# Kernel optimization log

Measured on AMD Instinct MI355X. Metric: run time of the kernel, lower is better.

## Reference

```python
import jax, jax.numpy as jnp
import numpy as np

N_HEAD = 4

def setup_inputs() -> dict:
    key = jax.random.key(0)
    ks = jax.random.split(key, 5)
    B, T, C = 2, 4096, 64
    return {
        "x": jax.random.normal(ks[0], (B, T, C), dtype=jnp.float32),
        "w_attn": jax.random.normal(ks[1], (3 * C, C), dtype=jnp.float32) * 0.02,
        "b_attn": jax.random.normal(ks[2], (3 * C,), dtype=jnp.float32) * 0.02,
        "w_proj": jax.random.normal(ks[3], (C, C), dtype=jnp.float32) * 0.02,
        "b_proj": jax.random.normal(ks[4], (C,), dtype=jnp.float32) * 0.02,
    }

def reference(x, w_attn, b_attn, w_proj, b_proj):
    B, T, C = x.shape
    H = N_HEAD
    Dh = C // H
    # fused QKV projection (torch Linear: x @ W.T + b)
    qkv = x @ w_attn.T + b_attn                      # [B,T,3C]
    q, k, v = jnp.split(qkv, 3, axis=-1)             # each [B,T,C]
    q = q.reshape(B, T, H, Dh).transpose(0, 2, 1, 3)  # [B,H,T,Dh]
    k = k.reshape(B, T, H, Dh).transpose(0, 2, 1, 3)
    v = v.reshape(B, T, H, Dh).transpose(0, 2, 1, 3)
    scale = 1.0 / np.sqrt(Dh).astype(np.float32)
    scores = jnp.einsum("bhqd,bhkd->bhqk", q, k) * scale  # [B,H,T,T]
    attn = jax.nn.softmax(scores, axis=-1)
    y = jnp.einsum("bhqk,bhkd->bhqd", attn, v)       # [B,H,T,Dh]
    y = y.transpose(0, 2, 1, 3).reshape(B, T, C)     # [B,T,C]
    return y @ w_proj.T + b_proj
```

## Files before the change

kernel.cpp:

```cpp
#include <hip/hip_runtime.h>
#include <math.h>

#define BB 2
#define TT 4096
#define CC 64
#define HH 4
#define DH 16
#define NROW (BB*TT)
#define SCALE 0.36067376022224085f

typedef __fp16 h4 __attribute__((ext_vector_type(4)));
typedef __fp16 h2 __attribute__((ext_vector_type(2)));
typedef float  f4 __attribute__((ext_vector_type(4)));

__global__ __launch_bounds__(256) void qkv_kernel(const float* __restrict__ x,
        const float* __restrict__ w, const float* __restrict__ bias,
        __fp16* __restrict__ Q, __fp16* __restrict__ K, __fp16* __restrict__ VT) {
    __shared__ __fp16 smv[64][16];
    const int t = threadIdx.x;
    const int wave = t >> 6, lane = t & 63;
    const int lq = lane & 15, g = lane >> 4;
    const int r0 = blockIdx.x*16;
    const int b = r0 >> 12, tt0 = r0 & (TT-1);

    h4 xb[4];
    const float* xrow = x + (size_t)(r0 + lq)*CC;
    #pragma unroll
    for (int s = 0; s < 4; s++) {
        float4 xv = *(const float4*)(xrow + s*16 + g*4);
        h2 lo = __builtin_amdgcn_cvt_pkrtz(xv.x, xv.y);
        h2 hi = __builtin_amdgcn_cvt_pkrtz(xv.z, xv.w);
        xb[s] = (h4){lo.x, lo.y, hi.x, hi.y};
    }

    #pragma unroll
    for (int j = 0; j < 3; j++) {
        const int nt = wave*3 + j;
        const int o0 = nt*16;
        const float sc = (nt < 4) ? SCALE : 1.0f;
        float4 bv = *(const float4*)(bias + o0 + g*4);
        f4 acc = {bv.x*sc, bv.y*sc, bv.z*sc, bv.w*sc};
        #pragma unroll
        for (int s = 0; s < 4; s++) {
            float4 wv = *(const float4*)(w + (size_t)(o0 + lq)*CC + s*16 + g*4);
            h2 lo = __builtin_amdgcn_cvt_pkrtz(wv.x*sc, wv.y*sc);
            h2 hi = __builtin_amdgcn_cvt_pkrtz(wv.z*sc, wv.w*sc);
            h4 af = (h4){lo.x, lo.y, hi.x, hi.y};
            acc = __builtin_amdgcn_mfma_f32_16x16x16f16(af, xb[s], acc, 0, 0, 0);
        }
        h2 plo = __builtin_amdgcn_cvt_pkrtz(acc.x, acc.y);
        h2 phi = __builtin_amdgcn_cvt_pkrtz(acc.z, acc.w);
        h4 pk = (h4){plo.x, plo.y, phi.x, phi.y};
        if (nt < 8) {
            const int part = nt >> 2, h = nt & 3;
            __fp16* dst = (part == 0) ? Q : K;
            *(h4*)(dst + ((size_t)(b*HH + h)*TT + tt0 + lq)*DH + g*4) = pk;
        } else {
            const int h = nt - 8;
            smv[h*16 + g*4 + 0][lq] = pk.x;
            smv[h*16 + g*4 + 1][lq] = pk.y;
            smv[h*16 + g*4 + 2][lq] = pk.z;
            smv[h*16 + g*4 + 3][lq] = pk.w;
        }
    }
    __syncthreads();
    if (t < 64) {
        const int h = t >> 4, d = t & 15;
        uint4 v0 = *(const uint4*)&smv[t][0];
        uint4 v1 = *(const uint4*)&smv[t][8];
        __fp16* dst = VT + (size_t)(b*HH + h)*TT*DH
                        + (size_t)((tt0 >> 6)*16 + d)*64 + (tt0 & 63);
        *(uint4*)dst = v0;
        *(uint4*)(dst + 8) = v1;
    }
}

__global__ __launch_bounds__(256) void attn_kernel(const __fp16* __restrict__ Q,
        const __fp16* __restrict__ K, const __fp16* __restrict__ VT,
        __fp16* __restrict__ yh) {
    __shared__ f4    Osm[4][4][64];
    __shared__ float Lsm[4][4][64];
    const int t = threadIdx.x;
    const int wave = t >> 6, lane = t & 63;
    const int lq = lane & 15, g = lane >> 4;
    const int head = blockIdx.x >> 6;
    const int qt   = blockIdx.x & 63;
    const int q0 = qt*64;
    const __fp16* Qh = Q  + (size_t)head*TT*DH;
    const __fp16* Kh = K  + (size_t)head*TT*DH;
    const __fp16* Vh = VT + (size_t)head*TT*DH;

    h4 qf[4];
    #pragma unroll
    for (int h = 0; h < 4; h++)
        qf[h] = *(const h4*)(Qh + (size_t)(q0 + h*16 + lq)*DH + g*4);

    f4 O[4];
    float lp[4];
    #pragma unroll
    for (int h = 0; h < 4; h++) { O[h] = (f4){0.f,0.f,0.f,0.f}; lp[h] = 0.f; }

    const __fp16* kp = Kh + (size_t)(wave*1024 + lq)*DH + g*4;
    const __fp16* vp = Vh + (size_t)(wave*16)*1024 + lq*64 + g*4;

    h4 ka[4], va[4], kb[4], vb[4];
    #pragma unroll
    for (int s = 0; s < 4; s++) {
        ka[s] = *(const h4*)(kp + (size_t)s*16*DH);
        va[s] = *(const h4*)(vp + s*16);
    }

#define ATTN_CHUNK(KF, VF)                                                        \
    {                                                                             \
        const f4 z = {0.f, 0.f, 0.f, 0.f};                                        \
        _Pragma("unroll")                                                         \
        for (int h = 0; h < 4; h++) {                                             \
            f4 S0 = __builtin_amdgcn_mfma_f32_16x16x16f16(KF[0], qf[h], z, 0,0,0);\
            f4 S1 = __builtin_amdgcn_mfma_f32_16x16x16f16(KF[1], qf[h], z, 0,0,0);\
            f4 S2 = __builtin_amdgcn_mfma_f32_16x16x16f16(KF[2], qf[h], z, 0,0,0);\
            f4 S3 = __builtin_amdgcn_mfma_f32_16x16x16f16(KF[3], qf[h], z, 0,0,0);\
            float p0, p1, p2, p3; h2 lo, hi; h4 P; float lacc = 0.f;              \
            p0 = __builtin_amdgcn_exp2f(S0.x); p1 = __builtin_amdgcn_exp2f(S0.y); \
            p2 = __builtin_amdgcn_exp2f(S0.z); p3 = __builtin_amdgcn_exp2f(S0.w); \
            lacc += p0 + p1 + p2 + p3;                                            \
            lo = __builtin_amdgcn_cvt_pkrtz(p0, p1);                              \
            hi = __builtin_amdgcn_cvt_pkrtz(p2, p3);                              \
            P = (h4){lo.x, lo.y, hi.x, hi.y};                                     \
            O[h] = __builtin_amdgcn_mfma_f32_16x16x16f16(VF[0], P, O[h], 0,0,0);  \
            p0 = __builtin_amdgcn_exp2f(S1.x); p1 = __builtin_amdgcn_exp2f(S1.y); \
            p2 = __builtin_amdgcn_exp2f(S1.z); p3 = __builtin_amdgcn_exp2f(S1.w); \
            lacc += p0 + p1 + p2 + p3;                                            \
            lo = __builtin_amdgcn_cvt_pkrtz(p0, p1);                              \
            hi = __builtin_amdgcn_cvt_pkrtz(p2, p3);                              \
            P = (h4){lo.x, lo.y, hi.x, hi.y};                                     \
            O[h] = __builtin_amdgcn_mfma_f32_16x16x16f16(VF[1], P, O[h], 0,0,0);  \
            p0 = __builtin_amdgcn_exp2f(S2.x); p1 = __builtin_amdgcn_exp2f(S2.y); \
            p2 = __builtin_amdgcn_exp2f(S2.z); p3 = __builtin_amdgcn_exp2f(S2.w); \
            lacc += p0 + p1 + p2 + p3;                                            \
            lo = __builtin_amdgcn_cvt_pkrtz(p0, p1);                              \
            hi = __builtin_amdgcn_cvt_pkrtz(p2, p3);                              \
            P = (h4){lo.x, lo.y, hi.x, hi.y};                                     \
            O[h] = __builtin_amdgcn_mfma_f32_16x16x16f16(VF[2], P, O[h], 0,0,0);  \
            p0 = __builtin_amdgcn_exp2f(S3.x); p1 = __builtin_amdgcn_exp2f(S3.y); \
            p2 = __builtin_amdgcn_exp2f(S3.z); p3 = __builtin_amdgcn_exp2f(S3.w); \
            lacc += p0 + p1 + p2 + p3;                                            \
            lo = __builtin_amdgcn_cvt_pkrtz(p0, p1);                              \
            hi = __builtin_amdgcn_cvt_pkrtz(p2, p3);                              \
            P = (h4){lo.x, lo.y, hi.x, hi.y};                                     \
            O[h] = __builtin_amdgcn_mfma_f32_16x16x16f16(VF[3], P, O[h], 0,0,0);  \
            lp[h] += lacc;                                                        \
        }                                                                         \
    }

    for (int step = 0; step < 16; step += 2) {
        {
            const __fp16* kp1 = kp + (size_t)(step + 1)*64*DH;
            const __fp16* vp1 = vp + (size_t)(step + 1)*1024;
            #pragma unroll
            for (int s = 0; s < 4; s++) {
                kb[s] = *(const h4*)(kp1 + (size_t)s*16*DH);
                vb[s] = *(const h4*)(vp1 + s*16);
            }
        }
        ATTN_CHUNK(ka, va)
        {
            const int c2 = (step + 2 < 16) ? step + 2 : 15;
            const __fp16* kp2 = kp + (size_t)c2*64*DH;
            const __fp16* vp2 = vp + (size_t)c2*1024;
            #pragma unroll
            for (int s = 0; s < 4; s++) {
                ka[s] = *(const h4*)(kp2 + (size_t)s*16*DH);
                va[s] = *(const h4*)(vp2 + s*16);
            }
        }
        ATTN_CHUNK(kb, vb)
    }
#undef ATTN_CHUNK

    #pragma unroll
    for (int h = 0; h < 4; h++) {
        Osm[wave][h][lane] = O[h];
        Lsm[wave][h][lane] = lp[h];
    }
    __syncthreads();

    f4 Os = Osm[0][wave][lane];
    Os += Osm[1][wave][lane];
    Os += Osm[2][wave][lane];
    Os += Osm[3][wave][lane];
    float L = 0.f;
    #pragma unroll
    for (int ks = 0; ks < 4; ks++)
        #pragma unroll
        for (int gg = 0; gg < 4; gg++)
            L += Lsm[ks][wave][gg*16 + lq];
    const float rinv = 1.f / L;
    h2 lo = __builtin_amdgcn_cvt_pkrtz(Os.x*rinv, Os.y*rinv);
    h2 hi = __builtin_amdgcn_cvt_pkrtz(Os.z*rinv, Os.w*rinv);
    h4 pk = (h4){lo.x, lo.y, hi.x, hi.y};
    const int b = head >> 2, hh = head & 3;
    *(h4*)(yh + ((size_t)b*TT + q0 + wave*16 + lq)*CC + hh*DH + g*4) = pk;
}

__global__ __launch_bounds__(256) void proj_kernel(const __fp16* __restrict__ yh,
        const float* __restrict__ w, const float* __restrict__ bias,
        float* __restrict__ out) {
    const int t = threadIdx.x;
    const int wave = t >> 6, lane = t & 63;
    const int lq = lane & 15, g = lane >> 4;
    const int r0 = blockIdx.x*16;

    h4 ya[4];
    const __fp16* yrow = yh + (size_t)(r0 + lq)*CC;
    #pragma unroll
    for (int ks = 0; ks < 4; ks++) ya[ks] = *(const h4*)(yrow + ks*16 + g*4);

    const int o = wave*16 + lq;
    const float bv = bias[o];
    f4 acc = {bv, bv, bv, bv};
    #pragma unroll
    for (int ks = 0; ks < 4; ks++) {
        float4 wv = *(const float4*)(w + (size_t)o*CC + ks*16 + g*4);
        h2 lo = __builtin_amdgcn_cvt_pkrtz(wv.x, wv.y);
        h2 hi = __builtin_amdgcn_cvt_pkrtz(wv.z, wv.w);
        h4 bf = (h4){lo.x, lo.y, hi.x, hi.y};
        acc = __builtin_amdgcn_mfma_f32_16x16x16f16(ya[ks], bf, acc, 0, 0, 0);
    }
    #pragma unroll
    for (int reg = 0; reg < 4; reg++)
        out[(size_t)(r0 + g*4 + reg)*CC + o] = acc[reg];
}

extern "C" void kernel_launch(void* const* d_in, const int* in_sizes, int n_in,
                              void* d_out, int out_size, void* d_ws, size_t ws_size,
                              hipStream_t stream) {
    const float* x      = (const float*)d_in[0];
    const float* w_attn = (const float*)d_in[1];
    const float* b_attn = (const float*)d_in[2];
    const float* w_proj = (const float*)d_in[3];
    const float* b_proj = (const float*)d_in[4];
    float* out = (float*)d_out;

    const size_t headsz = (size_t)BB*HH*TT*DH;
    __fp16* Q   = (__fp16*)d_ws;
    __fp16* K   = Q + headsz;
    __fp16* VT  = K + headsz;
    __fp16* yh  = VT + headsz;

    qkv_kernel<<<NROW/16, 256, 0, stream>>>(x, w_attn, b_attn, Q, K, VT);
    attn_kernel<<<BB*HH*(TT/64), 256, 0, stream>>>(Q, K, VT, yh);
    proj_kernel<<<NROW/16, 256, 0, stream>>>(yh, w_proj, b_proj, out);
}
```

Before: 95.33 us.

## Split attention key range across eight waves and vectorize projection output stores

Result: no change. 95.94 us (+0.6%).

```diff
diff --git a/kernel.cpp b/kernel.cpp
--- a/kernel.cpp
+++ b/kernel.cpp
@@ -75,7 +75,7 @@
     }
 }
 
-__global__ __launch_bounds__(256) void attn_kernel(const __fp16* __restrict__ Q,
+__global__ __launch_bounds__(512) void attn_kernel(const __fp16* __restrict__ Q,
         const __fp16* __restrict__ K, const __fp16* __restrict__ VT,
         __fp16* __restrict__ yh) {
     __shared__ f4    Osm[4][4][64];
@@ -100,8 +100,8 @@
     #pragma unroll
     for (int h = 0; h < 4; h++) { O[h] = (f4){0.f,0.f,0.f,0.f}; lp[h] = 0.f; }
 
-    const __fp16* kp = Kh + (size_t)(wave*1024 + lq)*DH + g*4;
-    const __fp16* vp = Vh + (size_t)(wave*16)*1024 + lq*64 + g*4;
+    const __fp16* kp = Kh + (size_t)(wave*512 + lq)*DH + g*4;
+    const __fp16* vp = Vh + (size_t)(wave*8)*1024 + lq*64 + g*4;
 
     h4 ka[4], va[4], kb[4], vb[4];
     #pragma unroll
@@ -152,7 +152,7 @@
         }                                                                         \
     }
 
-    for (int step = 0; step < 16; step += 2) {
+    for (int step = 0; step < 8; step += 2) {
         {
             const __fp16* kp1 = kp + (size_t)(step + 1)*64*DH;
             const __fp16* vp1 = vp + (size_t)(step + 1)*1024;
@@ -164,7 +164,7 @@
         }
         ATTN_CHUNK(ka, va)
         {
-            const int c2 = (step + 2 < 16) ? step + 2 : 15;
+            const int c2 = (step + 2 < 8) ? step + 2 : 7;
             const __fp16* kp2 = kp + (size_t)c2*64*DH;
             const __fp16* vp2 = vp + (size_t)c2*1024;
             #pragma unroll
@@ -177,29 +177,48 @@
     }
 #undef ATTN_CHUNK
 
-    #pragma unroll
-    for (int h = 0; h < 4; h++) {
-        Osm[wave][h][lane] = O[h];
-        Lsm[wave][h][lane] = lp[h];
-    }
-    __syncthreads();
-
-    f4 Os = Osm[0][wave][lane];
-    Os += Osm[1][wave][lane];
-    Os += Osm[2][wave][lane];
-    Os += Osm[3][wave][lane];
-    float L = 0.f;
-    #pragma unroll
-    for (int ks = 0; ks < 4; ks++)
-        #pragma unroll
-        for (int gg = 0; gg < 4; gg++)
-            L += Lsm[ks][wave][gg*16 + lq];
-    const float rinv = 1.f / L;
-    h2 lo = __builtin_amdgcn_cvt_pkrtz(Os.x*rinv, Os.y*rinv);
-    h2 hi = __builtin_amdgcn_cvt_pkrtz(Os.z*rinv, Os.w*rinv);
-    h4 pk = (h4){lo.x, lo.y, hi.x, hi.y};
-    const int b = head >> 2, hh = head & 3;
-    *(h4*)(yh + ((size_t)b*TT + q0 + wave*16 + lq)*CC + hh*DH + g*4) = pk;
+    if (wave >= 4) {
+        #pragma unroll
+        for (int h = 0; h < 4; h++) {
+            Osm[wave-4][h][lane] = O[h];
+            Lsm[wave-4][h][lane] = lp[h];
+        }
+    }
+    __syncthreads();
+    if (wave < 4) {
+        #pragma unroll
+        for (int h = 0; h < 4; h++) {
+            O[h] += Osm[wave][h][lane];
+            lp[h] += Lsm[wave][h][lane];
+        }
+    }
+    __syncthreads();
+    if (wave < 4) {
+        #pragma unroll
+        for (int h = 0; h < 4; h++) {
+            Osm[wave][h][lane] = O[h];
+            Lsm[wave][h][lane] = lp[h];
+        }
+    }
+    __syncthreads();
+    if (wave < 4) {
+        f4 Os = Osm[0][wave][lane];
+        Os += Osm[1][wave][lane];
+        Os += Osm[2][wave][lane];
+        Os += Osm[3][wave][lane];
+        float L = 0.f;
+        #pragma unroll
+        for (int ks = 0; ks < 4; ks++)
+            #pragma unroll
+            for (int gg = 0; gg < 4; gg++)
+                L += Lsm[ks][wave][gg*16 + lq];
+        const float rinv = 1.f / L;
+        h2 lo = __builtin_amdgcn_cvt_pkrtz(Os.x*rinv, Os.y*rinv);
+        h2 hi = __builtin_amdgcn_cvt_pkrtz(Os.z*rinv, Os.w*rinv);
+        h4 pk = (h4){lo.x, lo.y, hi.x, hi.y};
+        const int b = head >> 2, hh = head & 3;
+        *(h4*)(yh + ((size_t)b*TT + q0 + wave*16 + lq)*CC + hh*DH + g*4) = pk;
+    }
 }
 
 __global__ __launch_bounds__(256) void proj_kernel(const __fp16* __restrict__ yh,
@@ -209,26 +228,24 @@
     const int wave = t >> 6, lane = t & 63;
     const int lq = lane & 15, g = lane >> 4;
     const int r0 = blockIdx.x*16;
-
-    h4 ya[4];
+    const int o0 = wave*16;
+
+    h4 yb[4];
     const __fp16* yrow = yh + (size_t)(r0 + lq)*CC;
     #pragma unroll
-    for (int ks = 0; ks < 4; ks++) ya[ks] = *(const h4*)(yrow + ks*16 + g*4);
-
-    const int o = wave*16 + lq;
-    const float bv = bias[o];
-    f4 acc = {bv, bv, bv, bv};
-    #pragma unroll
-    for (int ks = 0; ks < 4; ks++) {
-        float4 wv = *(const float4*)(w + (size_t)o*CC + ks*16 + g*4);
+    for (int s = 0; s < 4; s++) yb[s] = *(const h4*)(yrow + s*16 + g*4);
+
+    float4 bv = *(const float4*)(bias + o0 + g*4);
+    f4 acc = {bv.x, bv.y, bv.z, bv.w};
+    #pragma unroll
+    for (int s = 0; s < 4; s++) {
+        float4 wv = *(const float4*)(w + (size_t)(o0 + lq)*CC + s*16 + g*4);
         h2 lo = __builtin_amdgcn_cvt_pkrtz(wv.x, wv.y);
         h2 hi = __builtin_amdgcn_cvt_pkrtz(wv.z, wv.w);
-        h4 bf = (h4){lo.x, lo.y, hi.x, hi.y};
-        acc = __builtin_amdgcn_mfma_f32_16x16x16f16(ya[ks], bf, acc, 0, 0, 0);
-    }
-    #pragma unroll
-    for (int reg = 0; reg < 4; reg++)
-        out[(size_t)(r0 + g*4 + reg)*CC + o] = acc[reg];
+        h4 af = (h4){lo.x, lo.y, hi.x, hi.y};
+        acc = __builtin_amdgcn_mfma_f32_16x16x16f16(af, yb[s], acc, 0, 0, 0);
+    }
+    *(float4*)(out + (size_t)(r0 + lq)*CC + o0 + g*4) = (float4){acc.x, acc.y, acc.z, acc.w};
 }
 
 extern "C" void kernel_launch(void* const* d_in, const int* in_sizes, int n_in,
@@ -248,6 +265,6 @@
     __fp16* yh  = VT + headsz;
 
     qkv_kernel<<<NROW/16, 256, 0, stream>>>(x, w_attn, b_attn, Q, K, VT);
-    attn_kernel<<<BB*HH*(TT/64), 256, 0, stream>>>(Q, K, VT, yh);
+    attn_kernel<<<BB*HH*(TT/64), 512, 0, stream>>>(Q, K, VT, yh);
     proj_kernel<<<NROW/16, 256, 0, stream>>>(yh, w_proj, b_proj, out);
 }
```
